# Kernel optimization log

Measured on AMD Instinct MI355X. Metric: run time of the kernel, lower is better.

## Reference

```python
import jax, jax.numpy as jnp
import numpy as np

EPS = 1e-5  # clamp floor in BitNet activation quantization


def _bitnet_act_quant(x):
    # Match transformers.integrations.bitnet.ActQuant: per-last-dim int8 fake-quant.
    scale = 127.0 / jnp.clip(jnp.max(jnp.abs(x), axis=-1, keepdims=True), EPS)
    return jnp.clip(jnp.round(x * scale), -128.0, 127.0) / scale


def setup_inputs() -> dict:
    key = jax.random.key(0)
    k1, k2, k3, k4 = jax.random.split(key, 4)
    B, S, D, O = 1, 4096, 4096, 4096  # batch, seq_len, in_features, out_features
    x = jax.random.normal(k1, (B, S, D), dtype=jnp.float32)
    # Ternary weight matrix in {-1, 0, +1} (what the bit-packed RSR format encodes).
    W = jax.random.randint(k2, (O, D), -1, 2).astype(jnp.float32)
    bias = jax.random.normal(k3, (O,), dtype=jnp.float32) * 0.01
    # BitNet weight_scale (divide mode): positive scalar.
    weight_scale = jax.random.uniform(k4, (), dtype=jnp.float32, minval=0.5, maxval=2.0)
    return {"x": x, "W": W, "bias": bias, "weight_scale": weight_scale}


def reference(x, W, bias, weight_scale):
    # CPU backend path: BitNet activation fake-quant, then ternary GEMV per token.
    q = _bitnet_act_quant(x.astype(jnp.float32))
    out = jnp.einsum('bsd,od->bso', q, W)  # [B, S, O]
    out = out + bias
    out = out / weight_scale  # weight_scale_mode == 'divide'
    return out.astype(x.dtype)
```

## Files before the change

kernel.cpp:

```cpp
#include <hip/hip_runtime.h>
#include <hip/hip_bf16.h>


#define SEQ  4096
#define DIM  4096
#define OUTD 4096

typedef int i32x4 __attribute__((ext_vector_type(4)));
typedef unsigned char u8;

__device__ __forceinline__ void gload16(const void* g, void* lds) {
    __builtin_amdgcn_global_load_lds(
        (const __attribute__((address_space(1))) void*)g,
        (__attribute__((address_space(3))) void*)lds, 16, 0, 0);
}

__device__ __forceinline__ int ldsoff(int r, int kq) {
    const int rp = r >> 1;
    const int w = (((r & 1) << 6) | (kq << 4)) ^ ((rp & 3) << 4);
    return rp * 128 + w;
}

__global__ __launch_bounds__(256) void prep_kernel(
    const float* __restrict__ x, char* __restrict__ q, float* __restrict__ rscale,
    const float4* __restrict__ W4, char4* __restrict__ Wb4) {
    const int bid = blockIdx.x;
    const int t = threadIdx.x;
    if (bid < SEQ) {
        const int row = bid;
        const int lane = t & 63, wave = t >> 6;
        const float4* xr = (const float4*)(x + (size_t)row * DIM);
        float4 r[4];
        float m = 0.0f;
#pragma unroll
        for (int i = 0; i < 4; ++i) {
            r[i] = xr[t + 256 * i];
            m = fmaxf(m, fmaxf(fmaxf(fabsf(r[i].x), fabsf(r[i].y)),
                               fmaxf(fabsf(r[i].z), fabsf(r[i].w))));
        }
#pragma unroll
        for (int off = 32; off > 0; off >>= 1)
            m = fmaxf(m, __shfl_xor(m, off, 64));
        __shared__ float red[4];
        if (lane == 0) red[wave] = m;
        __syncthreads();
        const float amax = fmaxf(fmaxf(red[0], red[1]), fmaxf(red[2], red[3]));
        const float scale = 127.0f / fmaxf(amax, 1e-5f);
        if (t == 0) rscale[row] = 1.0f / scale;
        char4* qr = (char4*)(q + (size_t)row * DIM);
#pragma unroll
        for (int i = 0; i < 4; ++i) {
            float q0 = fminf(127.0f, fmaxf(-128.0f, rintf(r[i].x * scale)));
            float q1 = fminf(127.0f, fmaxf(-128.0f, rintf(r[i].y * scale)));
            float q2 = fminf(127.0f, fmaxf(-128.0f, rintf(r[i].z * scale)));
            float q3 = fminf(127.0f, fmaxf(-128.0f, rintf(r[i].w * scale)));
            char4 o;
            o.x = (signed char)q0; o.y = (signed char)q1;
            o.z = (signed char)q2; o.w = (signed char)q3;
            qr[t + 256 * i] = o;
        }
    } else {
        const int n4 = (OUTD * DIM) / 4;
        int i = (bid - SEQ) * 256 + t;
        const int stride = SEQ * 256;
        for (; i < n4; i += stride) {
            float4 w = W4[i];
            char4 o;
            o.x = (signed char)w.x; o.y = (signed char)w.y;
            o.z = (signed char)w.z; o.w = (signed char)w.w;
            Wb4[i] = o;
        }
    }
}

__global__ __launch_bounds__(512, 2) void gemm_kernel(
    const u8* __restrict__ A, const u8* __restrict__ B,
    const float* __restrict__ rscale, const float* __restrict__ bias,
    const float* __restrict__ wscale, float* __restrict__ out) {
    __shared__ __align__(16) u8 As[4 * 16384];
    __shared__ __align__(16) u8 Bs[4 * 16384];
    const int tid = threadIdx.x;
    const int lane = tid & 63, wave = tid >> 6;
    const int wr = wave >> 2, wc = wave & 3;
    const int fr = lane & 15, kq = lane >> 4;

    const int bid = blockIdx.x;
    const int swz = (bid & 7) * 32 + (bid >> 3);
    const int brow = swz >> 4, bcol = swz & 15;

    const int v = (tid & 7) ^ ((tid >> 3) & 3);
    const int kb = (v & 3) * 16;
    const int r0 = ((tid >> 3) << 1) + (v >> 2);
    const u8* gA0 = A + (size_t)(brow * 256 + r0) * DIM + kb;
    const u8* gA1 = A + (size_t)(brow * 256 + 128 + r0) * DIM + kb;
    const u8* gB0 = B + (size_t)(bcol * 256 + r0) * DIM + kb;
    const u8* gB1 = B + (size_t)(bcol * 256 + 128 + r0) * DIM + kb;
    u8* lA0 = &As[tid * 16];
    u8* lA1 = &As[8192 + tid * 16];
    u8* lB0 = &Bs[tid * 16];
    u8* lB1 = &Bs[8192 + tid * 16];

#define STAGE(T, S) do { const int _k = (T) * 64;          \
        gload16(gA0 + _k, lA0 + (S) * 16384);              \
        gload16(gA1 + _k, lA1 + (S) * 16384);              \
        gload16(gB0 + _k, lB0 + (S) * 16384);              \
        gload16(gB1 + _k, lB1 + (S) * 16384); } while (0)

    int aoff[8], boff[4];
#pragma unroll
    for (int m = 0; m < 8; ++m) aoff[m] = ldsoff(wr * 128 + m * 16 + fr, kq);
#pragma unroll
    for (int n = 0; n < 4; ++n) boff[n] = ldsoff(wc * 64 + n * 16 + fr, kq);

    i32x4 acc[8][4] = {};

#define COMPUTE(S) do {                                                        \
        i32x4 af[8], bfv[4];                                                   \
        _Pragma("unroll")                                                      \
        for (int n = 0; n < 4; ++n)                                            \
            bfv[n] = *(const i32x4*)&Bs[(S) * 16384 + boff[n]];                \
        _Pragma("unroll")                                                      \
        for (int m = 0; m < 8; ++m)                                            \
            af[m] = *(const i32x4*)&As[(S) * 16384 + aoff[m]];                 \
        _Pragma("unroll")                                                      \
        for (int m = 0; m < 8; ++m)                                            \
            _Pragma("unroll")                                                  \
            for (int n = 0; n < 4; ++n)                                        \
                acc[m][n] = __builtin_amdgcn_mfma_i32_16x16x64_i8(             \
                    af[m], bfv[n], acc[m][n], 0, 0, 0);                        \
    } while (0)

#define VMW(N) asm volatile("s_waitcnt vmcnt(" #N ")" ::: "memory")
#define BAR()  do { asm volatile("" ::: "memory");                             \
                    __builtin_amdgcn_s_barrier();                              \
                    asm volatile("" ::: "memory"); } while (0)

    STAGE(0, 0); STAGE(1, 1); STAGE(2, 2);

    for (int tb = 0; tb < 15; ++tb) {
        const int t = tb * 4;
        VMW(8); BAR(); STAGE(t + 3, 3); COMPUTE(0);
        VMW(8); BAR(); STAGE(t + 4, 0); COMPUTE(1);
        VMW(8); BAR(); STAGE(t + 5, 1); COMPUTE(2);
        VMW(8); BAR(); STAGE(t + 6, 2); COMPUTE(3);
    }
    VMW(8); BAR(); STAGE(63, 3); COMPUTE(0);
    VMW(8); BAR(); COMPUTE(1);
    VMW(4); BAR(); COMPUTE(2);
    VMW(0); BAR(); COMPUTE(3);

    const float invws = 1.0f / wscale[0];
    const int rr0 = brow * 256 + wr * 128 + (kq << 2);
    const int c0 = bcol * 256 + wc * 64 + fr;
    float bv[4];
#pragma unroll
    for (int n = 0; n < 4; ++n) bv[n] = bias[c0 + n * 16] * invws;
#pragma unroll
    for (int m = 0; m < 8; ++m) {
#pragma unroll
        for (int j = 0; j < 4; ++j) {
            const int r = rr0 + m * 16 + j;
            const float rs = rscale[r] * invws;
            float* orow = out + (size_t)r * OUTD + c0;
#pragma unroll
            for (int n = 0; n < 4; ++n)
                orow[n * 16] = (float)acc[m][n][j] * rs + bv[n];
        }
    }
#undef STAGE
#undef COMPUTE
#undef VMW
#undef BAR
}

extern "C" void kernel_launch(void* const* d_in, const int* in_sizes, int n_in,
                              void* d_out, int out_size, void* d_ws, size_t ws_size,
                              hipStream_t stream) {
    const float* x      = (const float*)d_in[0];
    const float* W      = (const float*)d_in[1];
    const float* bias   = (const float*)d_in[2];
    const float* wscale = (const float*)d_in[3];
    float* out = (float*)d_out;

    char* ws = (char*)d_ws;
    char* q_i8 = ws;
    char* w_i8 = ws + (size_t)16777216;
    float* rscale = (float*)(ws + (size_t)33554432);

    prep_kernel<<<SEQ + 4096, 256, 0, stream>>>(
        x, q_i8, rscale, (const float4*)W, (char4*)w_i8);
    gemm_kernel<<<256, 512, 0, stream>>>((const u8*)q_i8, (const u8*)w_i8,
                                         rscale, bias, wscale, out);
}
```

Baseline: 91.51 us.

## Switch int8 GEMM to 32x32x32 MFMA with a new LDS tile layout

Replaces the 16x16x64 int8 MFMA tiles with 32x32x32 int8 MFMA. Each wave now holds a 4x2 grid of 32x32 accumulators instead of 8x4 of 16x16. The global-to-LDS load mapping and the LDS offsets are redone into a linear, unswizzled layout that matches the new fragment shape, and the epilogue is remapped to the 32x32 output register layout. The aim is fewer MFMA instructions and fewer LDS fragment reads per k-step. Dropping the XOR swizzle may bring back LDS bank conflicts.

```diff
diff --git a/kernel.cpp b/kernel.cpp
--- a/kernel.cpp
+++ b/kernel.cpp
@@ -7,18 +7,13 @@
 #define OUTD 4096
 
 typedef int i32x4 __attribute__((ext_vector_type(4)));
+typedef int i32x16 __attribute__((ext_vector_type(16)));
 typedef unsigned char u8;
 
 __device__ __forceinline__ void gload16(const void* g, void* lds) {
     __builtin_amdgcn_global_load_lds(
         (const __attribute__((address_space(1))) void*)g,
         (__attribute__((address_space(3))) void*)lds, 16, 0, 0);
-}
-
-__device__ __forceinline__ int ldsoff(int r, int kq) {
-    const int rp = r >> 1;
-    const int w = (((r & 1) << 6) | (kq << 4)) ^ ((rp & 3) << 4);
-    return rp * 128 + w;
 }
 
 __global__ __launch_bounds__(256) void prep_kernel(
@@ -82,19 +77,19 @@
     const int tid = threadIdx.x;
     const int lane = tid & 63, wave = tid >> 6;
     const int wr = wave >> 2, wc = wave & 3;
-    const int fr = lane & 15, kq = lane >> 4;
+    const int cl = lane & 31;
+    const int kh = lane >> 5;
 
     const int bid = blockIdx.x;
     const int swz = (bid & 7) * 32 + (bid >> 3);
     const int brow = swz >> 4, bcol = swz & 15;
 
-    const int v = (tid & 7) ^ ((tid >> 3) & 3);
-    const int kb = (v & 3) * 16;
-    const int r0 = ((tid >> 3) << 1) + (v >> 2);
-    const u8* gA0 = A + (size_t)(brow * 256 + r0) * DIM + kb;
-    const u8* gA1 = A + (size_t)(brow * 256 + 128 + r0) * DIM + kb;
-    const u8* gB0 = B + (size_t)(bcol * 256 + r0) * DIM + kb;
-    const u8* gB1 = B + (size_t)(bcol * 256 + 128 + r0) * DIM + kb;
+    const int rt = ((tid >> 7) << 5) + (tid & 31);
+    const int kbt = ((tid >> 5) & 3) * 16;
+    const u8* gA0 = A + (size_t)(brow * 256 + rt) * DIM + kbt;
+    const u8* gA1 = A + (size_t)(brow * 256 + 128 + rt) * DIM + kbt;
+    const u8* gB0 = B + (size_t)(bcol * 256 + rt) * DIM + kbt;
+    const u8* gB1 = B + (size_t)(bcol * 256 + 128 + rt) * DIM + kbt;
     u8* lA0 = &As[tid * 16];
     u8* lA1 = &As[8192 + tid * 16];
     u8* lB0 = &Bs[tid * 16];
@@ -106,28 +101,42 @@
         gload16(gB0 + _k, lB0 + (S) * 16384);              \
         gload16(gB1 + _k, lB1 + (S) * 16384); } while (0)
 
-    int aoff[8], boff[4];
-#pragma unroll
-    for (int m = 0; m < 8; ++m) aoff[m] = ldsoff(wr * 128 + m * 16 + fr, kq);
-#pragma unroll
-    for (int n = 0; n < 4; ++n) boff[n] = ldsoff(wc * 64 + n * 16 + fr, kq);
-
-    i32x4 acc[8][4] = {};
+    int aoff[4][2], boff[2][2];
+#pragma unroll
+    for (int m = 0; m < 4; ++m)
+#pragma unroll
+        for (int s = 0; s < 2; ++s)
+            aoff[m][s] = wr * 8192 + m * 2048 + s * 1024 + kh * 512 + cl * 16;
+#pragma unroll
+    for (int n = 0; n < 2; ++n)
+#pragma unroll
+        for (int s = 0; s < 2; ++s) {
+            const int bb = wc * 2 + n;
+            boff[n][s] = (bb >> 2) * 8192 + (bb & 3) * 2048 + s * 1024
+                         + kh * 512 + cl * 16;
+        }
+
+    i32x16 acc[4][2] = {};
 
 #define COMPUTE(S) do {                                                        \
-        i32x4 af[8], bfv[4];                                                   \
+        i32x4 af[4][2], bfv[2][2];                                             \
         _Pragma("unroll")                                                      \
-        for (int n = 0; n < 4; ++n)                                            \
-            bfv[n] = *(const i32x4*)&Bs[(S) * 16384 + boff[n]];                \
+        for (int s = 0; s < 2; ++s) {                                          \
+            _Pragma("unroll")                                                  \
+            for (int n = 0; n < 2; ++n)                                        \
+                bfv[n][s] = *(const i32x4*)&Bs[(S) * 16384 + boff[n][s]];      \
+            _Pragma("unroll")                                                  \
+            for (int m = 0; m < 4; ++m)                                        \
+                af[m][s] = *(const i32x4*)&As[(S) * 16384 + aoff[m][s]];       \
+        }                                                                      \
         _Pragma("unroll")                                                      \
-        for (int m = 0; m < 8; ++m)                                            \
-            af[m] = *(const i32x4*)&As[(S) * 16384 + aoff[m]];                 \
-        _Pragma("unroll")                                                      \
-        for (int m = 0; m < 8; ++m)                                            \
+        for (int s = 0; s < 2; ++s)                                            \
             _Pragma("unroll")                                                  \
-            for (int n = 0; n < 4; ++n)                                        \
-                acc[m][n] = __builtin_amdgcn_mfma_i32_16x16x64_i8(             \
-                    af[m], bfv[n], acc[m][n], 0, 0, 0);                        \
+            for (int m = 0; m < 4; ++m)                                        \
+                _Pragma("unroll")                                              \
+                for (int n = 0; n < 2; ++n)                                    \
+                    acc[m][n] = __builtin_amdgcn_mfma_i32_32x32x32_i8(         \
+                        af[m][s], bfv[n][s], acc[m][n], 0, 0, 0);              \
     } while (0)
 
 #define VMW(N) asm volatile("s_waitcnt vmcnt(" #N ")" ::: "memory")
@@ -150,21 +159,25 @@
     VMW(0); BAR(); COMPUTE(3);
 
     const float invws = 1.0f / wscale[0];
-    const int rr0 = brow * 256 + wr * 128 + (kq << 2);
-    const int c0 = bcol * 256 + wc * 64 + fr;
-    float bv[4];
-#pragma unroll
-    for (int n = 0; n < 4; ++n) bv[n] = bias[c0 + n * 16] * invws;
-#pragma unroll
-    for (int m = 0; m < 8; ++m) {
-#pragma unroll
-        for (int j = 0; j < 4; ++j) {
-            const int r = rr0 + m * 16 + j;
-            const float rs = rscale[r] * invws;
-            float* orow = out + (size_t)r * OUTD + c0;
-#pragma unroll
-            for (int n = 0; n < 4; ++n)
-                orow[n * 16] = (float)acc[m][n][j] * rs + bv[n];
+    const int rr0 = brow * 256 + wr * 128 + kh * 4;
+    const int c0 = bcol * 256 + wc * 64 + cl;
+    float bv[2];
+#pragma unroll
+    for (int n = 0; n < 2; ++n) bv[n] = bias[c0 + n * 32] * invws;
+#pragma unroll
+    for (int m = 0; m < 4; ++m) {
+#pragma unroll
+        for (int qg = 0; qg < 4; ++qg) {
+#pragma unroll
+            for (int j = 0; j < 4; ++j) {
+                const int r = rr0 + m * 32 + qg * 8 + j;
+                const int reg = qg * 4 + j;
+                const float rs = rscale[r] * invws;
+                float* orow = out + (size_t)r * OUTD + c0;
+#pragma unroll
+                for (int n = 0; n < 2; ++n)
+                    orow[n * 32] = (float)acc[m][n][reg] * rs + bv[n];
+            }
         }
     }
 #undef STAGE
```

New measurement: 101.5 us. +11.0%, slower.
